# Kernel optimization log

Measured on AMD Instinct MI355X. Metric: run time of the kernel, lower is better.

Reference implementation:

```python
import jax, jax.numpy as jnp
import numpy as np

NL, NH, H, FF, V, P = 12, 12, 768, 3072, 30522, 512
B, L, S = 4, 512, 8
DH = H // NH


def _layer_norm(x, g, b, eps=1e-12):
    m = x.mean(-1, keepdims=True)
    v = jnp.mean((x - m) ** 2, axis=-1, keepdims=True)
    return (x - m) * jax.lax.rsqrt(v + eps) * g + b


def setup_inputs() -> dict:
    key = jax.random.key(0)
    ks = iter(jax.random.split(key, 40))
    pm = lambda shape: jax.random.normal(next(ks), shape, jnp.float32) * 0.02
    inp = {
        'word_emb': pm((V, H)), 'pos_emb': pm((P, H)), 'type_emb': pm((2, H)),
        'emb_ln_g': jnp.ones((H,), jnp.float32), 'emb_ln_b': jnp.zeros((H,), jnp.float32),
        'Wq': pm((NL, H, H)), 'bq': jnp.zeros((NL, H), jnp.float32),
        'Wk': pm((NL, H, H)), 'bk': jnp.zeros((NL, H), jnp.float32),
        'Wv': pm((NL, H, H)), 'bv': jnp.zeros((NL, H), jnp.float32),
        'Wo': pm((NL, H, H)), 'bo': jnp.zeros((NL, H), jnp.float32),
        'attn_ln_g': jnp.ones((NL, H), jnp.float32), 'attn_ln_b': jnp.zeros((NL, H), jnp.float32),
        'W1': pm((NL, H, FF)), 'b1': jnp.zeros((NL, FF), jnp.float32),
        'W2': pm((NL, FF, H)), 'b2': jnp.zeros((NL, H), jnp.float32),
        'ffn_ln_g': jnp.ones((NL, H), jnp.float32), 'ffn_ln_b': jnp.zeros((NL, H), jnp.float32),
        'fc_w': pm((H,)), 'fc_b': jnp.zeros((), jnp.float32),
    }
    inp['input_ids'] = jax.random.randint(next(ks), (B, L), 0, V)
    inp['token_type_ids'] = jnp.zeros((B, L), jnp.int32)
    # valid-length prefix attention_mask and sorted bos_locations (history = 64)
    vl = np.array([384 + 16 * (i % 8) for i in range(B)])
    hist = 64
    am = (np.arange(L)[None, :] < vl[:, None]).astype(np.int32)
    bos = np.stack([hist + (np.arange(S) * (v - hist)) // S for v in vl]).astype(np.int64)
    inp['attention_mask'] = jnp.asarray(am)
    inp['bos_locations'] = jnp.asarray(bos)
    return inp


def _forward(word_emb, pos_emb, type_emb, emb_ln_g, emb_ln_b,
             Wq, bq, Wk, bk, Wv, bv, Wo, bo, attn_ln_g, attn_ln_b,
             W1, b1, W2, b2, ffn_ln_g, ffn_ln_b, fc_w, fc_b,
             input_ids, token_type_ids, attention_mask, bos_locations):
    Bs, Ls = input_ids.shape
    t = jnp.arange(Ls)
    valid_len = attention_mask.sum(-1)                       # [B]
    hist = bos_locations[:, 0]                               # [B] history length
    # segment id per token: number of bos positions <= t, minus 1 (-1 in history)
    seg = (bos_locations[:, :, None] <= t[None, None, :]).sum(1) - 1   # [B,L]
    valid = t[None, :] < valid_len[:, None]                  # [B,L]
    # block-diagonal candidate attention mask (history rows/cols fully visible)
    p = t[None, :, None]
    q = t[None, None, :]
    hist_pq = (p < hist[:, None, None]) | (q < hist[:, None, None])
    same_seg = seg[:, :, None] == seg[:, None, :]
    mask = valid[:, :, None] & valid[:, None, :] & (hist_pq | same_seg)  # [B,L,L]
    bias = jnp.where(mask, 0.0, -10000.0).astype(jnp.float32)[:, None, :, :]  # [B,1,L,L]

    # BERT embeddings
    x = word_emb[input_ids] + pos_emb[t][None] + type_emb[token_type_ids]
    x = _layer_norm(x, emb_ln_g, emb_ln_b)
    scale = 1.0 / jnp.sqrt(jnp.asarray(DH, x.dtype))

    for l in range(NL):
        qh = (x @ Wq[l] + bq[l]).reshape(Bs, Ls, NH, DH)
        kh = (x @ Wk[l] + bk[l]).reshape(Bs, Ls, NH, DH)
        vh = (x @ Wv[l] + bv[l]).reshape(Bs, Ls, NH, DH)
        scores = jnp.einsum('bqhd,bkhd->bhqk', qh, kh) * scale + bias
        probs = jax.nn.softmax(scores, axis=-1)
        ctx = jnp.einsum('bhqk,bkhd->bqhd', probs, vh).reshape(Bs, Ls, H)
        x = _layer_norm(x + ctx @ Wo[l] + bo[l], attn_ln_g[l], attn_ln_b[l])
        h = jax.nn.gelu(x @ W1[l] + b1[l], approximate=False)
        x = _layer_norm(x + h @ W2[l] + b2[l], ffn_ln_g[l], ffn_ln_b[l])

    # variable-length segment mean pooling via membership matmul
    starts = bos_locations                                   # [B,S]
    ends = jnp.concatenate([bos_locations[:, 1:], valid_len[:, None]], axis=1)
    memb = ((t[None, None, :] >= starts[:, :, None]) &
            (t[None, None, :] < ends[:, :, None])).astype(x.dtype)        # [B,S,L]
    pooled = jnp.einsum('bsl,bld->bsd', memb, x) / memb.sum(-1, keepdims=True)
    logits = pooled @ fc_w + fc_b                            # [B,S]
    return jnp.squeeze(logits)


def reference(word_emb, pos_emb, type_emb, emb_ln_g, emb_ln_b,
              Wq, bq, Wk, bk, Wv, bv, Wo, bo, attn_ln_g, attn_ln_b,
              W1, b1, W2, b2, ffn_ln_g, ffn_ln_b, fc_w, fc_b,
              input_ids, token_type_ids, attention_mask, bos_locations):
    return _forward(word_emb, pos_emb, type_emb, emb_ln_g, emb_ln_b,
                    Wq, bq, Wk, bk, Wv, bv, Wo, bo, attn_ln_g, attn_ln_b,
                    W1, b1, W2, b2, ffn_ln_g, ffn_ln_b, fc_w, fc_b,
                    input_ids, token_type_ids, attention_mask, bos_locations)
```

## Files before the change

### kernel.cpp

```cpp
#include <hip/hip_runtime.h>
#include <math.h>

#define HH 768
#define FF 3072
#define NL 12
#define NH 12
#define DH 64
#define BB 4
#define LL 512
#define SS 8
#define MM (BB*LL)
#define WQSZ (HH*HH)
#define W1SZ (HH*FF)
#define LWB 7077888
#define OFF_WO 1769472
#define OFF_W1 2359296
#define OFF_W2 4718592

typedef short bf16x8 __attribute__((ext_vector_type(8)));
typedef float f32x4 __attribute__((ext_vector_type(4)));

__device__ inline ushort f2b(float f) {
  unsigned u = __float_as_uint(f);
  unsigned r = (u + 0x7FFFu + ((u >> 16) & 1u)) >> 16;
  return (ushort)r;
}

__device__ inline void swz_xy(int& x, int& y) {
  int gx = gridDim.x, gy = gridDim.y;
  int flat = blockIdx.x + blockIdx.y * gx;
  int nwg = gx * gy;
  int q = nwg >> 3, r = nwg & 7;
  int xcd = flat & 7, off = flat >> 3;
  int wgid = (xcd < r ? xcd * (q + 1) : r * (q + 1) + (xcd - r) * q) + off;
  x = wgid / gy; y = wgid - x * gy;
}

__global__ void prep_kernel(const int* __restrict__ am, const int* __restrict__ bos,
                            int* __restrict__ seg, int* __restrict__ vl) {
  int b = blockIdx.x;
  int t = threadIdx.x;
  __shared__ int red[512];
  red[t] = am[b*LL + t];
  __syncthreads();
  for (int off = 256; off > 0; off >>= 1) {
    if (t < off) red[t] += red[t+off];
    __syncthreads();
  }
  if (t == 0) vl[b] = red[0];
  int cnt = 0;
  #pragma unroll
  for (int s = 0; s < SS; s++) cnt += (bos[b*SS + s] <= t) ? 1 : 0;
  seg[b*LL + t] = cnt - 1;
}

__global__ __launch_bounds__(256) void embed_ln_kernel(
    const float* __restrict__ word_emb, const float* __restrict__ pos_emb,
    const float* __restrict__ type_emb, const float* __restrict__ g,
    const float* __restrict__ bta, const int* __restrict__ ids,
    const int* __restrict__ tts, float* __restrict__ x, ushort* __restrict__ xb)
{
  int row = blockIdx.x;
  int l = row & (LL-1);
  int t = threadIdx.x;
  int id = ids[row];
  int ty = tts[row];
  float v[3];
  float s = 0.f, sq = 0.f;
  #pragma unroll
  for (int j = 0; j < 3; j++) {
    int c = t + j*256;
    float val = word_emb[(size_t)id*HH + c] + pos_emb[l*HH + c] + type_emb[ty*HH + c];
    v[j] = val; s += val; sq += val*val;
  }
  __shared__ float rs[256], rq[256];
  rs[t] = s; rq[t] = sq;
  __syncthreads();
  for (int off = 128; off > 0; off >>= 1) {
    if (t < off) { rs[t] += rs[t+off]; rq[t] += rq[t+off]; }
    __syncthreads();
  }
  float mean = rs[0] / HH;
  float var  = rq[0] / HH - mean*mean;
  float inv  = rsqrtf(var + 1e-12f);
  #pragma unroll
  for (int j = 0; j < 3; j++) {
    int c = t + j*256;
    float o = (v[j]-mean)*inv*g[c] + bta[c];
    x[(size_t)row*HH + c] = o;
    xb[(size_t)row*HH + c] = f2b(o);
  }
}

template<int NP>
__global__ __launch_bounds__(256) void add_ln_kernel(
    const float* __restrict__ xin, const float* __restrict__ y,
    const float* __restrict__ g, const float* __restrict__ bta,
    float* __restrict__ xout, ushort* __restrict__ xb)
{
  int row = blockIdx.x;
  int t = threadIdx.x;
  float v[3];
  float s = 0.f, sq = 0.f;
  #pragma unroll
  for (int j = 0; j < 3; j++) {
    int c = t + j*256;
    size_t ix = (size_t)row*HH + c;
    float val = xin[ix];
    #pragma unroll
    for (int p = 0; p < NP; p++) val += y[(size_t)p*MM*HH + ix];
    v[j] = val; s += val; sq += val*val;
  }
  __shared__ float rs[256], rq[256];
  rs[t] = s; rq[t] = sq;
  __syncthreads();
  for (int off = 128; off > 0; off >>= 1) {
    if (t < off) { rs[t] += rs[t+off]; rq[t] += rq[t+off]; }
    __syncthreads();
  }
  float mean = rs[0] / HH;
  float var  = rq[0] / HH - mean*mean;
  float inv  = rsqrtf(var + 1e-12f);
  #pragma unroll
  for (int j = 0; j < 3; j++) {
    int c = t + j*256;
    float o = (v[j]-mean)*inv*g[c] + bta[c];
    xout[(size_t)row*HH + c] = o;
    xb[(size_t)row*HH + c] = f2b(o);
  }
}

__global__ __launch_bounds__(256) void convw_all_kernel(
    const float* __restrict__ Wq, const float* __restrict__ Wk,
    const float* __restrict__ Wv, const float* __restrict__ Wo,
    const float* __restrict__ W1, const float* __restrict__ W2,
    ushort* __restrict__ wbuf)
{
  int idx = blockIdx.x;
  int l = idx / 432;
  int t0 = idx % 432;
  size_t base = (size_t)l * LWB;
  const float* src; ushort* dst; int Nsrc, dstK, k0b, n0src, n0dst;
  if (t0 < 108) {
    int nt = t0 / 3, ktg = t0 % 3;
    int z = nt / 12, ntl = nt % 12;
    src = (z == 0 ? Wq : z == 1 ? Wk : Wv) + (size_t)l*WQSZ;
    dst = wbuf + base;
    Nsrc = HH; dstK = HH; k0b = ktg*256; n0src = ntl*64; n0dst = nt*64;
  } else if (t0 < 144) {
    int t = t0 - 108; int nt = t / 3, ktg = t % 3;
    src = Wo + (size_t)l*WQSZ;
    dst = wbuf + base + OFF_WO;
    Nsrc = HH; dstK = HH; k0b = ktg*256; n0src = n0dst = nt*64;
  } else if (t0 < 288) {
    int t = t0 - 144; int nt = t / 3, ktg = t % 3;
    src = W1 + (size_t)l*W1SZ;
    dst = wbuf + base + OFF_W1;
    Nsrc = FF; dstK = HH; k0b = ktg*256; n0src = n0dst = nt*64;
  } else {
    int t = t0 - 288; int nt = t / 12, ktg = t % 12;
    src = W2 + (size_t)l*W1SZ;
    dst = wbuf + base + OFF_W2;
    Nsrc = HH; dstK = FF; k0b = ktg*256; n0src = n0dst = nt*64;
  }
  __shared__ ushort tt[4][64][66];
  int tid = threadIdx.x;
  int kr = tid >> 4;
  int nn0 = (tid & 15) << 2;
  #pragma unroll
  for (int ti = 0; ti < 4; ti++) {
    int k0 = k0b + ti*64;
    #pragma unroll
    for (int i = 0; i < 4; i++) {
      int k = kr + i*16;
      float4 v = *(const float4*)&src[(size_t)(k0+k)*Nsrc + n0src + nn0];
      ushort2 lo = { f2b(v.x), f2b(v.y) };
      ushort2 hi = { f2b(v.z), f2b(v.w) };
      *(ushort2*)&tt[ti][k][nn0]     = lo;
      *(ushort2*)&tt[ti][k][nn0 + 2] = hi;
    }
  }
  __syncthreads();
  #pragma unroll
  for (int it = 0; it < 2; it++) {
    int n  = it*32 + (tid >> 3);
    int kc = (tid & 7) << 3;
    #pragma unroll
    for (int ti = 0; ti < 4; ti++) {
      ushort tmp8[8];
      #pragma unroll
      for (int j = 0; j < 8; j++) tmp8[j] = tt[ti][kc + j][n];
      *(uint4*)&dst[(size_t)(n0dst + n)*dstK + k0b + ti*64 + kc] = *(const uint4*)tmp8;
    }
  }
}

template<int MODE>
__global__ __launch_bounds__(256) void gemm_bt(
    const ushort* __restrict__ A, const ushort* __restrict__ Bt,
    const float* __restrict__ ba, const float* __restrict__ bb,
    const float* __restrict__ bc, float* __restrict__ Cf,
    ushort* __restrict__ Cb, int M, int N, int K)
{
  __shared__ __align__(16) ushort As[2][128*64];
  __shared__ __align__(16) ushort Bs[2][64*64];
  const int tid = threadIdx.x;
  const int lane = tid & 63, wid = tid >> 6;
  const int wm = wid >> 1, wn = wid & 1;
  int bx, by; swz_xy(bx, by);
  const int m0 = by * 128, n0 = bx * 64;
  int kbeg = 0, kcnt = K;
  if (MODE == 2) { kcnt = K >> 2; kbeg = blockIdx.z * kcnt; }
  const int NT = kcnt >> 6;

  auto STAGE = [&](int buf, int k0) {
    #pragma unroll
    for (int j = 0; j < 4; j++) {
      int c = j*256 + tid;
      int r = c >> 3;
      int kk = ((c & 7) ^ (r & 7)) << 3;
      __builtin_amdgcn_global_load_lds(
        (const __attribute__((address_space(1))) void*)(A + (size_t)(m0+r)*K + k0 + kk),
        (__attribute__((address_space(3))) void*)(&As[buf][c*8]), 16, 0, 0);
    }
    #pragma unroll
    for (int j = 0; j < 2; j++) {
      int c = j*256 + tid;
      int r = c >> 3;
      int kk = ((c & 7) ^ (r & 7)) << 3;
      __builtin_amdgcn_global_load_lds(
        (const __attribute__((address_space(1))) void*)(Bt + (size_t)(n0+r)*K + k0 + kk),
        (__attribute__((address_space(3))) void*)(&Bs[buf][c*8]), 16, 0, 0);
    }
  };

  f32x4 acc[4][2] = {};
  STAGE(0, kbeg);
  __syncthreads();
  int cur = 0;
  for (int t = 0; t < NT; ++t) {
    if (t + 1 < NT) STAGE(cur ^ 1, kbeg + (t+1)*64);
    bf16x8 af[4][2], bfv[2][2];
    #pragma unroll
    for (int mi = 0; mi < 4; mi++) {
      int row = wm*64 + mi*16 + (lane & 15);
      #pragma unroll
      for (int ks = 0; ks < 2; ks++) {
        int kb = (ks*64 + ((lane >> 4) << 4)) ^ ((row & 7) << 4);
        af[mi][ks] = *(const bf16x8*)((const char*)&As[cur][0] + row*128 + kb);
      }
    }
    #pragma unroll
    for (int ni = 0; ni < 2; ni++) {
      int row = wn*32 + ni*16 + (lane & 15);
      #pragma unroll
      for (int ks = 0; ks < 2; ks++) {
        int kb = (ks*64 + ((lane >> 4) << 4)) ^ ((row & 7) << 4);
        bfv[ni][ks] = *(const bf16x8*)((const char*)&Bs[cur][0] + row*128 + kb);
      }
    }
    #pragma unroll
    for (int ks = 0; ks < 2; ks++)
      #pragma unroll
      for (int mi = 0; mi < 4; mi++)
        #pragma unroll
        for (int ni = 0; ni < 2; ni++)
          acc[mi][ni] = __builtin_amdgcn_mfma_f32_16x16x32_bf16(af[mi][ks], bfv[ni][ks], acc[mi][ni], 0, 0, 0);
    __syncthreads();
    cur ^= 1;
  }

  #pragma unroll
  for (int mi = 0; mi < 4; mi++) {
    #pragma unroll
    for (int ni = 0; ni < 2; ni++) {
      int col = n0 + wn*32 + ni*16 + (lane & 15);
      if (MODE == 0) {
        int z = n0 / 768;
        int cc = col - z*768;
        float bvv = (z == 0 ? ba : z == 1 ? bb : bc)[cc];
        #pragma unroll
        for (int r = 0; r < 4; r++) {
          int row = m0 + wm*64 + mi*16 + (lane >> 4)*4 + r;
          Cb[(size_t)z*MM*HH + (size_t)row*HH + cc] = f2b(acc[mi][ni][r] + bvv);
        }
      } else if (MODE == 1) {
        float bvv = ba[col];
        #pragma unroll
        for (int r = 0; r < 4; r++) {
          int row = m0 + wm*64 + mi*16 + (lane >> 4)*4 + r;
          float v = acc[mi][ni][r] + bvv;
          v = 0.5f * v * (1.0f + erff(v * 0.70710678118654752f));
          Cb[(size_t)row*N + col] = f2b(v);
        }
      } else {
        float bvv = (blockIdx.z == 0) ? ba[col] : 0.f;
        #pragma unroll
        for (int r = 0; r < 4; r++) {
          int row = m0 + wm*64 + mi*16 + (lane >> 4)*4 + r;
          Cf[(size_t)blockIdx.z*M*N + (size_t)row*N + col] = acc[mi][ni][r] + bvv;
        }
      }
    }
  }
}

__global__ __launch_bounds__(256) void attn_mfma_kernel(
    const ushort* __restrict__ Q, const ushort* __restrict__ Kp, const ushort* __restrict__ Vp,
    ushort* __restrict__ ctx, const int* __restrict__ seg, const int* __restrict__ vl,
    const int* __restrict__ bos)
{
  const int q0 = blockIdx.x * 64;
  const int h  = blockIdx.y;
  const int b  = blockIdx.z;
  const int tid = threadIdx.x;
  const int lane = tid & 63;
  const int wid = tid >> 6;

  __shared__ __align__(16) char Ks[2][8192];
  __shared__ __align__(16) char Vt[2][8192];
  __shared__ __align__(16) char Ps[4][2048];
  __shared__ int segk[2][64];

  const int qrow_frag = q0 + wid*16 + (lane & 15);
  bf16x8 qf[2];
  #pragma unroll
  for (int c = 0; c < 2; c++)
    qf[c] = *(const bf16x8*)&Q[((size_t)(b*LL + qrow_frag))*HH + h*DH + 32*c + (lane >> 4)*8];

  const int vlb  = vl[b];
  const int hist = bos[b*SS];
  int segq[4]; bool qvalid[4], qhist[4];
  #pragma unroll
  for (int r = 0; r < 4; r++) {
    int qg = q0 + wid*16 + (lane >> 4)*4 + r;
    segq[r]   = seg[b*LL + qg];
    qvalid[r] = qg < vlb;
    qhist[r]  = qg < hist;
  }

  float mrow[4], lrow[4];
  #pragma unroll
  for (int r = 0; r < 4; r++) { mrow[r] = -1e30f; lrow[r] = 0.f; }
  f32x4 Oacc[4] = {};

  uint4 kreg0, kreg1, vreg0, vreg1;
  int sreg = 0;

  auto LOADT = [&](int k0) {
    int rk = tid >> 3;
    int c8 = (tid & 7) * 8;
    kreg0 = *(const uint4*)&Kp[((size_t)(b*LL + k0 + rk))*HH + h*DH + c8];
    kreg1 = *(const uint4*)&Kp[((size_t)(b*LL + k0 + rk + 32))*HH + h*DH + c8];
    vreg0 = *(const uint4*)&Vp[((size_t)(b*LL + k0 + lane))*HH + h*DH + wid*8];
    vreg1 = *(const uint4*)&Vp[((size_t)(b*LL + k0 + lane))*HH + h*DH + wid*8 + 32];
    if (tid < 64) sreg = seg[b*LL + k0 + tid];
  };
  auto STORET = [&](int buf) {
    int rk = tid >> 3;
    int c8 = (tid & 7) * 8;
    *(uint4*)(Ks[buf] + (rk*128 + ((c8*2) ^ ((rk & 7) << 4)))) = kreg0;
    int rk2 = rk + 32;
    *(uint4*)(Ks[buf] + (rk2*128 + ((c8*2) ^ ((rk2 & 7) << 4)))) = kreg1;
    const ushort* pv0 = (const ushort*)&vreg0;
    const ushort* pv1 = (const ushort*)&vreg1;
    #pragma unroll
    for (int j = 0; j < 8; j++) {
      int d  = wid*8 + j;
      *(ushort*)(Vt[buf] + (d*128 + ((lane*2) ^ ((d & 7) << 4)))) = pv0[j];
      int d2 = d + 32;
      *(ushort*)(Vt[buf] + (d2*128 + ((lane*2) ^ ((d2 & 7) << 4)))) = pv1[j];
    }
    if (tid < 64) segk[buf][tid] = sreg;
  };

  LOADT(0);
  STORET(0);
  __syncthreads();

  for (int kt = 0; kt < 8; kt++) {
    const int cur = kt & 1;
    const int k0 = kt * 64;
    if (kt < 7) LOADT(k0 + 64);
    __builtin_amdgcn_sched_barrier(0);

    f32x4 sacc[4] = {};
    #pragma unroll
    for (int t = 0; t < 4; t++) {
      int krow = (lane & 15) + 16*t;
      #pragma unroll
      for (int c = 0; c < 2; c++) {
        bf16x8 kf = *(const bf16x8*)(Ks[cur] + (krow*128 +
                      (((32*c + (lane >> 4)*8)*2) ^ ((krow & 7) << 4))));
        sacc[t] = __builtin_amdgcn_mfma_f32_16x16x32_bf16(qf[c], kf, sacc[t], 0, 0, 0);
      }
    }

    #pragma unroll
    for (int t = 0; t < 4; t++) {
      int kg = k0 + (lane & 15) + 16*t;
      bool kvalid = kg < vlb;
      bool khist  = kg < hist;
      int  sk     = segk[cur][(lane & 15) + 16*t];
      #pragma unroll
      for (int r = 0; r < 4; r++) {
        bool ok = qvalid[r] && kvalid && (khist || qhist[r] || (segq[r] == sk));
        sacc[t][r] = sacc[t][r]*0.125f + (ok ? 0.f : -10000.f);
      }
    }

    float scl[4];
    #pragma unroll
    for (int r = 0; r < 4; r++) {
      float rm = fmaxf(fmaxf(sacc[0][r], sacc[1][r]), fmaxf(sacc[2][r], sacc[3][r]));
      rm = fmaxf(rm, __shfl_xor(rm, 1));
      rm = fmaxf(rm, __shfl_xor(rm, 2));
      rm = fmaxf(rm, __shfl_xor(rm, 4));
      rm = fmaxf(rm, __shfl_xor(rm, 8));
      float mnew = fmaxf(mrow[r], rm);
      scl[r] = __expf(mrow[r] - mnew);
      float rsum = 0.f;
      #pragma unroll
      for (int t = 0; t < 4; t++) {
        float p = __expf(sacc[t][r] - mnew);
        sacc[t][r] = p;
        rsum += p;
      }
      rsum += __shfl_xor(rsum, 1);
      rsum += __shfl_xor(rsum, 2);
      rsum += __shfl_xor(rsum, 4);
      rsum += __shfl_xor(rsum, 8);
      mrow[r] = mnew;
      lrow[r] = lrow[r]*scl[r] + rsum;
    }

    char* Pl = Ps[wid];
    #pragma unroll
    for (int t = 0; t < 4; t++) {
      #pragma unroll
      for (int r = 0; r < 4; r++) {
        int q = (lane >> 4)*4 + r;
        int k = (lane & 15) + 16*t;
        *(ushort*)(Pl + (q*128 + ((k*2) ^ ((q & 7) << 4)))) = f2b(sacc[t][r]);
      }
    }
    asm volatile("s_waitcnt lgkmcnt(0)" ::: "memory");
    bf16x8 pf[2];
    #pragma unroll
    for (int c = 0; c < 2; c++) {
      int q = lane & 15;
      int k = 32*c + (lane >> 4)*8;
      pf[c] = *(const bf16x8*)(Pl + (q*128 + ((k*2) ^ ((q & 7) << 4))));
    }

    #pragma unroll
    for (int nt = 0; nt < 4; nt++) {
      #pragma unroll
      for (int r = 0; r < 4; r++) Oacc[nt][r] *= scl[r];
      int d = (lane & 15) + 16*nt;
      #pragma unroll
      for (int c = 0; c < 2; c++) {
        int k = 32*c + (lane >> 4)*8;
        bf16x8 vf = *(const bf16x8*)(Vt[cur] + (d*128 + ((k*2) ^ ((d & 7) << 4))));
        Oacc[nt] = __builtin_amdgcn_mfma_f32_16x16x32_bf16(pf[c], vf, Oacc[nt], 0, 0, 0);
      }
    }

    if (kt < 7) STORET(cur ^ 1);
    __syncthreads();
  }

  #pragma unroll
  for (int nt = 0; nt < 4; nt++) {
    #pragma unroll
    for (int r = 0; r < 4; r++) {
      int q = q0 + wid*16 + (lane >> 4)*4 + r;
      int d = h*DH + (lane & 15) + 16*nt;
      ctx[(size_t)(b*LL + q)*HH + d] = f2b(Oacc[nt][r] / lrow[r]);
    }
  }
}

__global__ __launch_bounds__(256) void rowdot_kernel(const float* __restrict__ x,
                                                     const float* __restrict__ w,
                                                     float* __restrict__ rd) {
  int row = blockIdx.x;
  int t = threadIdx.x;
  float s = 0.f;
  #pragma unroll
  for (int j = 0; j < 3; j++) {
    int c = t + j*256;
    s = fmaf(x[(size_t)row*HH + c], w[c], s);
  }
  __shared__ float red[256];
  red[t] = s;
  __syncthreads();
  for (int off = 128; off > 0; off >>= 1) {
    if (t < off) red[t] += red[t+off];
    __syncthreads();
  }
  if (t == 0) rd[row] = red[0];
}

__global__ void logits_kernel(const float* __restrict__ rd, const int* __restrict__ bos,
                              const int* __restrict__ vl, const float* __restrict__ fcb,
                              float* __restrict__ out) {
  int i = threadIdx.x;
  if (i >= BB*SS) return;
  int b = i / SS, s = i % SS;
  int start = bos[b*SS + s];
  int end   = (s == SS-1) ? vl[b] : bos[b*SS + s + 1];
  float sum = 0.f;
  for (int t = start; t < end; t++) sum += rd[b*LL + t];
  out[i] = sum / (float)(end - start) + fcb[0];
}

extern "C" void kernel_launch(void* const* d_in, const int* in_sizes, int n_in,
                              void* d_out, int out_size, void* d_ws, size_t ws_size,
                              hipStream_t stream) {
  const float* word_emb  = (const float*)d_in[0];
  const float* pos_emb   = (const float*)d_in[1];
  const float* type_emb  = (const float*)d_in[2];
  const float* emb_ln_g  = (const float*)d_in[3];
  const float* emb_ln_b  = (const float*)d_in[4];
  const float* Wq        = (const float*)d_in[5];
  const float* bq        = (const float*)d_in[6];
  const float* Wk        = (const float*)d_in[7];
  const float* bk        = (const float*)d_in[8];
  const float* Wv        = (const float*)d_in[9];
  const float* bv        = (const float*)d_in[10];
  const float* Wo        = (const float*)d_in[11];
  const float* bo        = (const float*)d_in[12];
  const float* attn_ln_g = (const float*)d_in[13];
  const float* attn_ln_b = (const float*)d_in[14];
  const float* W1        = (const float*)d_in[15];
  const float* b1        = (const float*)d_in[16];
  const float* W2        = (const float*)d_in[17];
  const float* b2        = (const float*)d_in[18];
  const float* ffn_ln_g  = (const float*)d_in[19];
  const float* ffn_ln_b  = (const float*)d_in[20];
  const float* fc_w      = (const float*)d_in[21];
  const float* fc_b      = (const float*)d_in[22];
  const int* input_ids   = (const int*)d_in[23];
  const int* token_type  = (const int*)d_in[24];
  const int* am          = (const int*)d_in[25];
  const int* bos         = (const int*)d_in[26];
  float* out = (float*)d_out;

  char* w = (char*)d_ws;
  float*  x       = (float*)w;  w += (size_t)MM*HH*4;
  float*  tmp     = (float*)w;  w += (size_t)4*MM*HH*4;
  ushort* qkv_bf  = (ushort*)w; w += (size_t)3*MM*HH*2;
  ushort* x_bf    = (ushort*)w; w += (size_t)MM*HH*2;
  ushort* ctx_bf  = (ushort*)w; w += (size_t)MM*HH*2;
  ushort* hbuf_bf = (ushort*)w; w += (size_t)MM*FF*2;
  ushort* wbuf    = (ushort*)w; w += (size_t)NL*LWB*2;
  float*  rd      = (float*)w;  w += (size_t)MM*4;
  int*    seg     = (int*)w;    w += (size_t)MM*4;
  int*    vl      = (int*)w;    w += 64;

  prep_kernel<<<BB, 512, 0, stream>>>(am, bos, seg, vl);
  convw_all_kernel<<<NL*432, 256, 0, stream>>>(Wq, Wk, Wv, Wo, W1, W2, wbuf);
  embed_ln_kernel<<<MM, 256, 0, stream>>>(word_emb, pos_emb, type_emb,
                                          emb_ln_g, emb_ln_b, input_ids, token_type, x, x_bf);

  dim3 gqkv(2304/64, MM/128);
  dim3 g_ff1(FF/64, MM/128);
  dim3 g_sk(HH/64, MM/128, 4);
  dim3 gattn(LL/64, NH, BB);

  for (int l = 0; l < NL; l++) {
    const ushort* Wqkv_t = wbuf + (size_t)l*LWB;
    const ushort* Wo_t   = wbuf + (size_t)l*LWB + OFF_WO;
    const ushort* W1_t   = wbuf + (size_t)l*LWB + OFF_W1;
    const ushort* W2_t   = wbuf + (size_t)l*LWB + OFF_W2;

    gemm_bt<0><<<gqkv, 256, 0, stream>>>(x_bf, Wqkv_t,
        bq + (size_t)l*HH, bk + (size_t)l*HH, bv + (size_t)l*HH,
        nullptr, qkv_bf, MM, 2304, HH);

    attn_mfma_kernel<<<gattn, 256, 0, stream>>>(qkv_bf, qkv_bf + (size_t)MM*HH,
                                                qkv_bf + (size_t)2*MM*HH, ctx_bf, seg, vl, bos);

    gemm_bt<2><<<g_sk, 256, 0, stream>>>(ctx_bf, Wo_t,
        bo + (size_t)l*HH, nullptr, nullptr, tmp, nullptr, MM, HH, HH);

    add_ln_kernel<4><<<MM, 256, 0, stream>>>(x, tmp, attn_ln_g + (size_t)l*HH,
                                             attn_ln_b + (size_t)l*HH, x, x_bf);

    gemm_bt<1><<<g_ff1, 256, 0, stream>>>(x_bf, W1_t,
        b1 + (size_t)l*FF, nullptr, nullptr, nullptr, hbuf_bf, MM, FF, HH);

    gemm_bt<2><<<g_sk, 256, 0, stream>>>(hbuf_bf, W2_t,
        b2 + (size_t)l*HH, nullptr, nullptr, tmp, nullptr, MM, HH, FF);

    add_ln_kernel<4><<<MM, 256, 0, stream>>>(x, tmp, ffn_ln_g + (size_t)l*HH,
                                             ffn_ln_b + (size_t)l*HH, x, x_bf);
  }

  rowdot_kernel<<<MM, 256, 0, stream>>>(x, fc_w, rd);
  logits_kernel<<<1, 64, 0, stream>>>(rd, bos, vl, fc_b, out);
}
```

Before: 1.430 ms.

## Vectorize layernorm/rowdot loads and add lazy softmax rescaling in attention

The embed, add-layernorm and rowdot kernels switch from three strided scalar accesses per thread to one float4 load and store per thread, with 192 of 256 threads active. This cuts memory instruction count in these bandwidth-bound row kernels. Separately, the flash-attention online softmax only raises the running max when the new tile max exceeds the old one by more than 8, and skips the rescale of the output accumulator when no row needs it. That saves exp and multiply work but lets the exponentials run up to e^8 above the stored max, which is a numerics risk.

```diff
diff --git a/kernel.cpp b/kernel.cpp
--- a/kernel.cpp
+++ b/kernel.cpp
@@ -65,13 +65,16 @@
   int t = threadIdx.x;
   int id = ids[row];
   int ty = tts[row];
-  float v[3];
+  float4 v = {0.f,0.f,0.f,0.f};
   float s = 0.f, sq = 0.f;
-  #pragma unroll
-  for (int j = 0; j < 3; j++) {
-    int c = t + j*256;
-    float val = word_emb[(size_t)id*HH + c] + pos_emb[l*HH + c] + type_emb[ty*HH + c];
-    v[j] = val; s += val; sq += val*val;
+  int c = t << 2;
+  if (t < 192) {
+    float4 a = *(const float4*)&word_emb[(size_t)id*HH + c];
+    float4 p = *(const float4*)&pos_emb[l*HH + c];
+    float4 ttv = *(const float4*)&type_emb[ty*HH + c];
+    v.x = a.x+p.x+ttv.x; v.y = a.y+p.y+ttv.y; v.z = a.z+p.z+ttv.z; v.w = a.w+p.w+ttv.w;
+    s = v.x+v.y+v.z+v.w;
+    sq = v.x*v.x+v.y*v.y+v.z*v.z+v.w*v.w;
   }
   __shared__ float rs[256], rq[256];
   rs[t] = s; rq[t] = sq;
@@ -83,12 +86,17 @@
   float mean = rs[0] / HH;
   float var  = rq[0] / HH - mean*mean;
   float inv  = rsqrtf(var + 1e-12f);
-  #pragma unroll
-  for (int j = 0; j < 3; j++) {
-    int c = t + j*256;
-    float o = (v[j]-mean)*inv*g[c] + bta[c];
-    x[(size_t)row*HH + c] = o;
-    xb[(size_t)row*HH + c] = f2b(o);
+  if (t < 192) {
+    float4 gv = *(const float4*)&g[c];
+    float4 bv = *(const float4*)&bta[c];
+    float4 o;
+    o.x = (v.x-mean)*inv*gv.x + bv.x;
+    o.y = (v.y-mean)*inv*gv.y + bv.y;
+    o.z = (v.z-mean)*inv*gv.z + bv.z;
+    o.w = (v.w-mean)*inv*gv.w + bv.w;
+    *(float4*)&x[(size_t)row*HH + c] = o;
+    ushort4 ob = { f2b(o.x), f2b(o.y), f2b(o.z), f2b(o.w) };
+    *(ushort4*)&xb[(size_t)row*HH + c] = ob;
   }
 }
 
@@ -100,16 +108,19 @@
 {
   int row = blockIdx.x;
   int t = threadIdx.x;
-  float v[3];
+  float4 v = {0.f,0.f,0.f,0.f};
   float s = 0.f, sq = 0.f;
-  #pragma unroll
-  for (int j = 0; j < 3; j++) {
-    int c = t + j*256;
-    size_t ix = (size_t)row*HH + c;
-    float val = xin[ix];
-    #pragma unroll
-    for (int p = 0; p < NP; p++) val += y[(size_t)p*MM*HH + ix];
-    v[j] = val; s += val; sq += val*val;
+  int c = t << 2;
+  size_t ix = (size_t)row*HH + c;
+  if (t < 192) {
+    v = *(const float4*)&xin[ix];
+    #pragma unroll
+    for (int p = 0; p < NP; p++) {
+      float4 yv = *(const float4*)&y[(size_t)p*MM*HH + ix];
+      v.x += yv.x; v.y += yv.y; v.z += yv.z; v.w += yv.w;
+    }
+    s = v.x+v.y+v.z+v.w;
+    sq = v.x*v.x+v.y*v.y+v.z*v.z+v.w*v.w;
   }
   __shared__ float rs[256], rq[256];
   rs[t] = s; rq[t] = sq;
@@ -121,12 +132,17 @@
   float mean = rs[0] / HH;
   float var  = rq[0] / HH - mean*mean;
   float inv  = rsqrtf(var + 1e-12f);
-  #pragma unroll
-  for (int j = 0; j < 3; j++) {
-    int c = t + j*256;
-    float o = (v[j]-mean)*inv*g[c] + bta[c];
-    xout[(size_t)row*HH + c] = o;
-    xb[(size_t)row*HH + c] = f2b(o);
+  if (t < 192) {
+    float4 gv = *(const float4*)&g[c];
+    float4 bv = *(const float4*)&bta[c];
+    float4 o;
+    o.x = (v.x-mean)*inv*gv.x + bv.x;
+    o.y = (v.y-mean)*inv*gv.y + bv.y;
+    o.z = (v.z-mean)*inv*gv.z + bv.z;
+    o.w = (v.w-mean)*inv*gv.w + bv.w;
+    *(float4*)&xout[ix] = o;
+    ushort4 ob = { f2b(o.x), f2b(o.y), f2b(o.z), f2b(o.w) };
+    *(ushort4*)&xb[ix] = ob;
   }
 }
 
@@ -417,8 +433,8 @@
       rm = fmaxf(rm, __shfl_xor(rm, 2));
       rm = fmaxf(rm, __shfl_xor(rm, 4));
       rm = fmaxf(rm, __shfl_xor(rm, 8));
-      float mnew = fmaxf(mrow[r], rm);
-      scl[r] = __expf(mrow[r] - mnew);
+      float mnew = (rm > mrow[r] + 8.f) ? rm : mrow[r];
+      scl[r] = (mnew == mrow[r]) ? 1.f : __expf(mrow[r] - mnew);
       float rsum = 0.f;
       #pragma unroll
       for (int t = 0; t < 4; t++) {
@@ -453,10 +469,13 @@
       pf[c] = *(const bf16x8*)(Pl + (q*128 + ((k*2) ^ ((q & 7) << 4))));
     }
 
+    bool needscale = (scl[0] != 1.f) | (scl[1] != 1.f) | (scl[2] != 1.f) | (scl[3] != 1.f);
     #pragma unroll
     for (int nt = 0; nt < 4; nt++) {
-      #pragma unroll
-      for (int r = 0; r < 4; r++) Oacc[nt][r] *= scl[r];
+      if (needscale) {
+        #pragma unroll
+        for (int r = 0; r < 4; r++) Oacc[nt][r] *= scl[r];
+      }
       int d = (lane & 15) + 16*nt;
       #pragma unroll
       for (int c = 0; c < 2; c++) {
@@ -487,10 +506,11 @@
   int row = blockIdx.x;
   int t = threadIdx.x;
   float s = 0.f;
-  #pragma unroll
-  for (int j = 0; j < 3; j++) {
-    int c = t + j*256;
-    s = fmaf(x[(size_t)row*HH + c], w[c], s);
+  if (t < 192) {
+    int c = t << 2;
+    float4 xv = *(const float4*)&x[(size_t)row*HH + c];
+    float4 wv = *(const float4*)&w[c];
+    s = xv.x*wv.x + xv.y*wv.y + xv.z*wv.z + xv.w*wv.w;
   }
   __shared__ float red[256];
   red[t] = s;
```

New measurement: 1.429 ms. About the same (-0.1%).
